# Performance work log

Hardware: AMD Instinct MI355X
Metric: run time of the kernel (lower is better)

## Reference

```python
import jax, jax.numpy as jnp
import numpy as np
from jax import lax

C = 128      # channels
H = 128
W = 128
B = 2
WS = 4       # window size
HEADS = 4
HID = int(C * 2.66)  # 340
EPS = 1e-6


def conv1x1(x, w):
    # x: [b,c,h,w], w: [out,in]
    return jnp.einsum('oc,bchw->bohw', w, x)


def dwconv3(x, w):
    # depthwise 3x3, w: [c,1,3,3]
    return lax.conv_general_dilated(
        x, w, window_strides=(1, 1), padding='SAME',
        feature_group_count=x.shape[1],
        dimension_numbers=('NCHW', 'OIHW', 'NCHW'))


def layernorm(x, w, b):
    # channel-wise LN over dim 1 (per pixel), w/b: [C]
    m = x.mean(axis=1, keepdims=True)
    v = ((x - m) ** 2).mean(axis=1, keepdims=True)
    xn = (x - m) / jnp.sqrt(v + EPS)
    return xn * w[None, :, None, None] + b[None, :, None, None]


def l2norm(x):
    n = jnp.sqrt(jnp.sum(x * x, axis=-1, keepdims=True))
    return x / jnp.maximum(n, 1e-12)


def rsa(x, qkv_w, dw_w, proj_w, temp):
    b, c, h, w = x.shape
    ws = WS
    x_ = jnp.roll(x, (-ws // 2, -ws // 2), axis=(2, 3))  # shifts > 0
    qkv = dwconv3(conv1x1(x_, qkv_w), dw_w)
    q, k, v = jnp.split(qkv, 3, axis=1)

    def win(t):  # b c (h dh) (w dw) -> b (h w) (dh dw) c
        return t.reshape(b, c, h // ws, ws, w // ws, ws) \
                .transpose(0, 2, 4, 3, 5, 1) \
                .reshape(b, (h // ws) * (w // ws), ws * ws, c)

    q, k, v = win(q), win(k), win(v)
    q = l2norm(q)
    k = l2norm(k)
    # attn = q^T @ k  -> [b, nw, c, c]
    attn = jax.nn.relu(jnp.einsum('bnpc,bnpd->bncd', q, k) * temp[0, 0, 0])
    out = jnp.einsum('bnpc,bncd->bnpd', v, attn)  # v @ attn
    out = out.reshape(b, h // ws, w // ws, ws, ws, c) \
             .transpose(0, 5, 1, 3, 2, 4).reshape(b, c, h, w)
    out = jnp.roll(out, (ws // 2, ws // 2), axis=(2, 3))
    return conv1x1(out, proj_w)


def gsa(x, qkv_w, dw_w, proj_w, temp):
    b, c, h, w = x.shape
    hd = HEADS
    ch = c // hd
    qkv = dwconv3(conv1x1(x, qkv_w), dw_w)
    q, k, v = jnp.split(qkv, 3, axis=1)

    def hs(t):  # b (head c) h w -> b head c (h w)
        return t.reshape(b, hd, ch, h * w)

    q, k, v = hs(q), hs(k), hs(v)
    q = l2norm(q)
    k = l2norm(k)
    attn = jax.nn.relu(jnp.einsum('bhcn,bhdn->bhcd', q, k) * temp[0, 0, 0])
    out = jnp.einsum('bhcd,bhdn->bhcn', attn, v).reshape(b, c, h, w)
    return conv1x1(out, proj_w)


def ffn(x, w_in, w_dw, w_out):
    h = dwconv3(conv1x1(x, w_in), w_dw)
    h = jax.nn.gelu(h, approximate=False)
    return conv1x1(h, w_out)


def setup_inputs() -> dict:
    key = jax.random.key(0)
    ks = jax.random.split(key, 16)
    s = 0.05
    d = {
        'x': jax.random.normal(ks[0], (B, C, H, W), jnp.float32),
        # spatial (RSA) branch
        'w_s0': jnp.ones((C,), jnp.float32), 'b_s0': jnp.zeros((C,), jnp.float32),
        'w_s2': jnp.ones((C,), jnp.float32), 'b_s2': jnp.zeros((C,), jnp.float32),
        'rsa_qkv': jax.random.normal(ks[1], (3 * C, C), jnp.float32) * s,
        'rsa_dw': jax.random.normal(ks[2], (3 * C, 1, 3, 3), jnp.float32) * s,
        'rsa_proj': jax.random.normal(ks[3], (C, C), jnp.float32) * s,
        'rsa_temp': jnp.ones((1, 1, 1), jnp.float32),
        'ffs_in': jax.random.normal(ks[4], (HID, C), jnp.float32) * s,
        'ffs_dw': jax.random.normal(ks[5], (HID, 1, 3, 3), jnp.float32) * s,
        'ffs_out': jax.random.normal(ks[6], (C, HID), jnp.float32) * s,
        # channel (GSA) branch
        'w_c0': jnp.ones((C,), jnp.float32), 'b_c0': jnp.zeros((C,), jnp.float32),
        'w_c2': jnp.ones((C,), jnp.float32), 'b_c2': jnp.zeros((C,), jnp.float32),
        'gsa_qkv': jax.random.normal(ks[7], (3 * C, C), jnp.float32) * s,
        'gsa_dw': jax.random.normal(ks[8], (3 * C, 1, 3, 3), jnp.float32) * s,
        'gsa_proj': jax.random.normal(ks[9], (C, C), jnp.float32) * s,
        'gsa_temp': jnp.ones((1, 1, 1), jnp.float32),
        'ffc_in': jax.random.normal(ks[10], (HID, C), jnp.float32) * s,
        'ffc_dw': jax.random.normal(ks[11], (HID, 1, 3, 3), jnp.float32) * s,
        'ffc_out': jax.random.normal(ks[12], (C, HID), jnp.float32) * s,
    }
    return d


def reference(x, w_s0, b_s0, w_s2, b_s2, rsa_qkv, rsa_dw, rsa_proj, rsa_temp,
              ffs_in, ffs_dw, ffs_out,
              w_c0, b_c0, w_c2, b_c2, gsa_qkv, gsa_dw, gsa_proj, gsa_temp,
              ffc_in, ffc_dw, ffc_out):
    # shared_depth = 1: only the i==0 branches execute
    # spatial block (RSA)
    x_ = rsa(layernorm(x, w_s0, b_s0), rsa_qkv, rsa_dw, rsa_proj, rsa_temp)
    x = ffn(layernorm(x_ + x, w_s2, b_s2), ffs_in, ffs_dw, ffs_out) + x_
    # channel block (GSA)
    x_ = gsa(layernorm(x, w_c0, b_c0), gsa_qkv, gsa_dw, gsa_proj, gsa_temp)
    x = ffn(layernorm(x_ + x, w_c2, b_c2), ffc_in, ffc_dw, ffc_out) + x_
    return x
```

## Files before the change

### kernel.cpp

```cpp
#include <hip/hip_runtime.h>
#include <hip/hip_bf16.h>
#include <math.h>

typedef __hip_bfloat16 bf16;
typedef __attribute__((ext_vector_type(8))) short short8;
typedef __attribute__((ext_vector_type(4))) short short4v;
typedef __attribute__((ext_vector_type(4))) float float4v;

static constexpr int cB  = 2;
static constexpr int cC  = 128;
static constexpr int cH  = 128;
static constexpr int cW  = 128;
static constexpr int cP  = cH * cW;
static constexpr int cC3 = 384;
static constexpr int cHID = 340;
static constexpr int cNW = 1024;
static constexpr float cEPS = 1e-6f;

__device__ __forceinline__ float bfu2f(unsigned short u){
  union { unsigned int i; float f; } c; c.i = ((unsigned int)u) << 16; return c.f;
}
__device__ __forceinline__ unsigned short f2b(float f){
  union { float f; unsigned int u; } c; c.f = f;
  unsigned int r = c.u + 0x7FFFu + ((c.u >> 16) & 1u);
  return (unsigned short)(r >> 16);
}

__global__ void k_wcvt(const float* __restrict__ qkv_s, const float* __restrict__ qkv_c,
                       const float* __restrict__ fin_s, const float* __restrict__ fin_c,
                       const float* __restrict__ prj_s, const float* __restrict__ prj_c,
                       const float* __restrict__ fo_s,  const float* __restrict__ fo_c,
                       unsigned short* __restrict__ WB, float* __restrict__ S){
  int i = blockIdx.x * 256 + threadIdx.x;
  if (i >= 319488){
    int j = i - 319488;
    if (j < 8704) S[j] = 0.f;
    return;
  }
  float v;
  if (i < 98304){
    v = (i < 49152) ? qkv_s[i] : qkv_c[i - 49152];
  } else if (i < 196608){
    int j = (i < 147456) ? (i - 98304) : (i - 147456);
    int row = j >> 7, col = j & 127;
    const float* src = (i < 147456) ? fin_s : fin_c;
    v = (row < cHID) ? src[row * 128 + col] : 0.f;
  } else if (i < 229376){
    v = (i < 212992) ? prj_s[i - 196608] : prj_c[i - 212992];
  } else {
    int j = (i < 274432) ? (i - 229376) : (i - 274432);
    int row = j / 352, col = j - row * 352;
    const float* src = (i < 274432) ? fo_s : fo_c;
    v = (col < cHID) ? src[row * cHID + col] : 0.f;
  }
  WB[i] = f2b(v);
}

__global__ void __launch_bounds__(256) k_ln(const float* __restrict__ a,
                                            const float* __restrict__ gamma,
                                            const float* __restrict__ beta,
                                            unsigned short* __restrict__ out, int sh, int sw){
  int idx = blockIdx.x * 256 + threadIdx.x;
  if (idx >= cB * cP) return;
  int b = idx >> 14;
  int p = idx & (cP - 1);
  const float* ap = a + (size_t)b * cC * cP + p;
  float s = 0.f, ss = 0.f;
  #pragma unroll 8
  for (int c = 0; c < cC; c++){
    float v = ap[c * cP];
    s += v; ss += v * v;
  }
  float m = s * (1.f / cC);
  float var = ss * (1.f / cC) - m * m;
  float rstd = rsqrtf(var + cEPS);
  int h = p >> 7, w = p & 127;
  int h2 = (h + sh) & (cH - 1);
  int w2 = (w + sw) & (cW - 1);
  unsigned short* op = out + (size_t)b * cP * cC + (size_t)(h2 * cW + w2) * cC;
  #pragma unroll
  for (int c8 = 0; c8 < cC; c8 += 8){
    short8 tv;
    #pragma unroll
    for (int j = 0; j < 8; j++){
      float v = ap[(c8 + j) * cP];
      tv[j] = (short)f2b((v - m) * rstd * gamma[c8 + j] + beta[c8 + j]);
    }
    *(short8*)(op + c8) = tv;
  }
}

__global__ void __launch_bounds__(256) k_gemm(const unsigned short* __restrict__ Wb,
                                              const unsigned short* __restrict__ Xg,
                                              unsigned short* __restrict__ Out,
                                              int K, int PK, int PM){
  __shared__ short SMEM[8704];
  short* Wls = SMEM;
  short* Xls = SMEM + 5120;
  int bid = blockIdx.x;
  int s  = (bid & 7) * (1536 >> 3) + (bid >> 3);
  int mt = s % 3;
  int r3 = s / 3;
  int pt = r3 & 255;
  int b  = r3 >> 8;
  int p0 = pt * 64;
  int m0 = mt * 128;
  int t  = threadIdx.x;
  int lanelo = t & 15;
  int quad   = (t >> 4) & 3;
  int wv = t >> 6;
  int w1 = wv & 1;
  int w2 = wv >> 1;
  int srw = t >> 1;
  int kow = (t & 1) * 16;
  int srx = t >> 2;
  int kox = (t & 3) * 8;

  float4v acc[2][4];
  #pragma unroll
  for (int i = 0; i < 2; i++)
    #pragma unroll
    for (int j = 0; j < 4; j++)
      acc[i][j] = (float4v){0.f, 0.f, 0.f, 0.f};

  const unsigned short* Xb = Xg + (size_t)b * cP * PK;

  for (int k0 = 0; k0 < K; k0 += 32){
    short8 xv  = *(const short8*)(Xb + (size_t)(p0 + srx) * PK + k0 + kox);
    short8 wv0 = *(const short8*)(Wb + (size_t)(m0 + srw) * K + k0 + kow);
    short8 wv1 = *(const short8*)(Wb + (size_t)(m0 + srw) * K + k0 + kow + 8);
    __syncthreads();
    *(short8*)&Wls[srw * 40 + kow]     = wv0;
    *(short8*)&Wls[srw * 40 + kow + 8] = wv1;
    *(short8*)&Xls[srx * 40 + kox]     = xv;
    __syncthreads();
    short8 af[2], bfr[4];
    #pragma unroll
    for (int i = 0; i < 2; i++)
      af[i] = *(const short8*)&Xls[(w1 * 32 + i * 16 + lanelo) * 40 + quad * 8];
    #pragma unroll
    for (int j = 0; j < 4; j++)
      bfr[j] = *(const short8*)&Wls[(w2 * 64 + j * 16 + lanelo) * 40 + quad * 8];
    #pragma unroll
    for (int i = 0; i < 2; i++)
      #pragma unroll
      for (int j = 0; j < 4; j++)
        acc[i][j] = __builtin_amdgcn_mfma_f32_16x16x32_bf16(af[i], bfr[j], acc[i][j], 0, 0, 0);
  }
  __syncthreads();
  #pragma unroll
  for (int i = 0; i < 2; i++)
    #pragma unroll
    for (int j = 0; j < 4; j++){
      int pixloc = w1 * 32 + i * 16 + quad * 4;
      int mloc   = w2 * 64 + j * 16 + lanelo;
      #pragma unroll
      for (int r = 0; r < 4; r++)
        SMEM[(pixloc + r) * 136 + mloc] = (short)f2b(acc[i][j][r]);
    }
  __syncthreads();
  unsigned short* Ob = Out + (size_t)b * cP * PM;
  #pragma unroll
  for (int rr = 0; rr < 4; rr++){
    int id = t + rr * 256;
    int row = id >> 4, col8 = (id & 15) * 8;
    int wcol = m0 + col8;
    if (wcol < PM)
      *(short8*)(Ob + (size_t)(p0 + row) * PM + wcol) = *(const short8*)&SMEM[row * 136 + col8];
  }
}

template<int MODE>
__global__ void __launch_bounds__(256) k_gemm64(const unsigned short* __restrict__ Wb,
                                                const unsigned short* __restrict__ Xg,
                                                const float* __restrict__ R,
                                                const float* __restrict__ Base,
                                                const float* __restrict__ gamma,
                                                const float* __restrict__ beta,
                                                float* __restrict__ Tr,
                                                unsigned short* __restrict__ LNo,
                                                int K, int PK){
  __shared__ short SMEM[8704];
  __shared__ float gls[128], bls[128];
  __shared__ float psum[64], pssq[64];
  short* Wls = SMEM;
  short* Xls = SMEM + 5120;
  int b  = blockIdx.z;
  int p0 = blockIdx.x * 64;
  int t  = threadIdx.x;
  int lanelo = t & 15;
  int quad   = (t >> 4) & 3;
  int wv = t >> 6;
  int w2 = wv >> 1, w1 = wv & 1;
  int srw = t >> 1;
  int kow = (t & 1) * 16;
  int srx = t >> 2;
  int kox = (t & 3) * 8;

  if (MODE != 3){
    if (t < 128){ gls[t] = gamma[t]; bls[t] = beta[t]; }
    if (t < 64){ psum[t] = 0.f; pssq[t] = 0.f; }
  }

  float4v acc[4][2];
  #pragma unroll
  for (int i = 0; i < 4; i++){
    acc[i][0] = (float4v){0.f, 0.f, 0.f, 0.f};
    acc[i][1] = (float4v){0.f, 0.f, 0.f, 0.f};
  }
  const unsigned short* Xb = Xg + (size_t)b * cP * PK;

  for (int k0 = 0; k0 < K; k0 += 32){
    short8 xv = *(const short8*)(Xb + (size_t)(p0 + srx) * PK + k0 + kox);
    short8 wv0 = *(const short8*)(Wb + (size_t)srw * K + k0 + kow);
    short8 wv1 = *(const short8*)(Wb + (size_t)srw * K + k0 + kow + 8);
    __syncthreads();
    *(short8*)&Wls[srw * 40 + kow]     = wv0;
    *(short8*)&Wls[srw * 40 + kow + 8] = wv1;
    *(short8*)&Xls[srx * 40 + kox]     = xv;
    __syncthreads();
    short8 af[4], bfr[2];
    #pragma unroll
    for (int i = 0; i < 4; i++)
      af[i] = *(const short8*)&Wls[(w2 * 64 + i * 16 + lanelo) * 40 + quad * 8];
    #pragma unroll
    for (int j = 0; j < 2; j++)
      bfr[j] = *(const short8*)&Xls[(w1 * 32 + j * 16 + lanelo) * 40 + quad * 8];
    #pragma unroll
    for (int i = 0; i < 4; i++)
      #pragma unroll
      for (int j = 0; j < 2; j++)
        acc[i][j] = __builtin_amdgcn_mfma_f32_16x16x32_bf16(af[i], bfr[j], acc[i][j], 0, 0, 0);
  }
  float lnv[4][2][4];
  #pragma unroll
  for (int i = 0; i < 4; i++)
    #pragma unroll
    for (int j = 0; j < 2; j++){
      int n = p0 + w1 * 32 + j * 16 + lanelo;
      #pragma unroll
      for (int r = 0; r < 4; r++){
        int m = w2 * 64 + i * 16 + quad * 4 + r;
        size_t idx = (size_t)b * cC * cP + (size_t)m * cP + n;
        float v = acc[i][j][r];
        if (MODE >= 2) v += R[idx];
        Tr[idx] = v;
        if (MODE == 1) v += Base[idx];
        lnv[i][j][r] = v;
      }
    }
  if (MODE == 3) return;
  __syncthreads();
  #pragma unroll
  for (int j = 0; j < 2; j++){
    int nl = w1 * 32 + j * 16 + lanelo;
    float s = 0.f, ss = 0.f;
    #pragma unroll
    for (int i = 0; i < 4; i++)
      #pragma unroll
      for (int r = 0; r < 4; r++){
        float v = lnv[i][j][r];
        s += v; ss += v * v;
      }
    atomicAdd(&psum[nl], s);
    atomicAdd(&pssq[nl], ss);
  }
  __syncthreads();
  #pragma unroll
  for (int j = 0; j < 2; j++){
    int nl = w1 * 32 + j * 16 + lanelo;
    float mean = psum[nl] * (1.f / cC);
    float var = pssq[nl] * (1.f / cC) - mean * mean;
    float rstd = rsqrtf(var + cEPS);
    #pragma unroll
    for (int i = 0; i < 4; i++)
      #pragma unroll
      for (int r = 0; r < 4; r++){
        int m = w2 * 64 + i * 16 + quad * 4 + r;
        SMEM[nl * 136 + m] = (short)f2b((lnv[i][j][r] - mean) * rstd * gls[m] + bls[m]);
      }
  }
  __syncthreads();
  unsigned short* Ob = LNo + (size_t)b * cP * cC;
  #pragma unroll
  for (int rr = 0; rr < 4; rr++){
    int id = t + rr * 256;
    int row = id >> 4, col8 = (id & 15) * 8;
    short8 sv = *(const short8*)&SMEM[row * 136 + col8];
    *(short8*)(Ob + (size_t)(p0 + row) * cC + col8) = sv;
  }
}

template<int GELU, int CCn, int PITCH>
__global__ void __launch_bounds__(256) k_dw(const unsigned short* __restrict__ in,
                                            const float* __restrict__ wt,
                                            unsigned short* __restrict__ out){
  __shared__ float wls[16 * 76];
  int t = threadIdx.x;
  int cbase = blockIdx.y * 128;
  for (int i = t; i < 16 * 72; i += 256){
    int cg = i / 72, rem = i - cg * 72;
    int tap = rem >> 3, j = rem & 7;
    int c = cbase + cg * 8 + j;
    wls[cg * 76 + rem] = (c < CCn) ? wt[c * 9 + tap] : 0.f;
  }
  __syncthreads();
  int cgl = t & 15, pixl = t >> 4;
  int c0 = cbase + cgl * 8;
  if (c0 >= PITCH) return;
  int p = blockIdx.x * 16 + pixl;
  int h = p >> 7, w = p & 127;
  int b = blockIdx.z;
  const unsigned short* ib = in + (size_t)b * cP * PITCH;
  float4 wreg[18];
  #pragma unroll
  for (int q = 0; q < 18; q++)
    wreg[q] = *(const float4*)&wls[cgl * 76 + q * 4];
  short8 v[9];
  #pragma unroll
  for (int ky = 0; ky < 3; ky++){
    int hh = h + ky - 1;
    bool okh = (unsigned)hh < (unsigned)cH;
    int hc = okh ? hh : h;
    #pragma unroll
    for (int kx = 0; kx < 3; kx++){
      int ww = w + kx - 1;
      bool okw = (unsigned)ww < (unsigned)cW;
      int wc = okw ? ww : w;
      short8 lv = *(const short8*)(ib + (size_t)(hc * cW + wc) * PITCH + c0);
      if (!(okh && okw)) lv = (short8){0,0,0,0,0,0,0,0};
      v[ky * 3 + kx] = lv;
    }
  }
  float acc[8] = {0,0,0,0,0,0,0,0};
  #pragma unroll
  for (int tap = 0; tap < 9; tap++){
    float4 w0 = wreg[tap * 2];
    float4 w1 = wreg[tap * 2 + 1];
    float wa[8] = {w0.x, w0.y, w0.z, w0.w, w1.x, w1.y, w1.z, w1.w};
    #pragma unroll
    for (int j = 0; j < 8; j++)
      acc[j] += wa[j] * bfu2f((unsigned short)v[tap][j]);
  }
  short8 ov;
  #pragma unroll
  for (int j = 0; j < 8; j++){
    float vv = acc[j];
    if (GELU) vv = 0.5f * vv * (1.f + erff(vv * 0.70710678118654752f));
    ov[j] = (short)f2b(vv);
  }
  *(short8*)(out + (size_t)b * cP * PITCH + (size_t)p * PITCH + c0) = ov;
}

__global__ void __launch_bounds__(256) k_rsa(const unsigned short* __restrict__ qkv,
                                             const float* __restrict__ temp,
                                             unsigned short* __restrict__ out){
  constexpr int QT = 0;
  constexpr int KT = 5120;
  constexpr int VO = 10240;
  constexpr int AT = 12416;
  __shared__ short lds[21632];
  __shared__ float nq[16], nk[16];
  int blk = blockIdx.x;
  int b  = blk >> 10;
  int nw = blk & 1023;
  int hb = nw >> 5, wb = nw & 31;
  int t = threadIdx.x;
  #pragma unroll
  for (int j = 0; j < 5; j++)
    *(short8*)&lds[t * 40 + j * 8] = (short8){0,0,0,0,0,0,0,0};
  if (t < 16) nq[t] = 0.f;
  else if (t < 32) nk[t - 16] = 0.f;
  __syncthreads();
  const unsigned short* base = qkv + (size_t)b * cP * cC3;
  #pragma unroll
  for (int r = 0; r < 3; r++){
    int i = t + 256 * r;
    int pix = i / 48;
    int cg = i - pix * 48;
    int c0 = cg * 8;
    int gp = (hb * 4 + (pix >> 2)) * cW + wb * 4 + (pix & 3);
    short8 v = *(const short8*)(base + (size_t)gp * cC3 + c0);
    if (c0 < 256){
      float s = 0.f;
      #pragma unroll
      for (int e = 0; e < 8; e++){ float f = bfu2f((unsigned short)v[e]); s += f * f; }
      int off = (c0 < 128) ? (QT + c0 * 40) : (KT + (c0 - 128) * 40);
      #pragma unroll
      for (int e = 0; e < 8; e++) lds[off + e * 40 + pix] = v[e];
      atomicAdd((c0 < 128) ? &nq[pix] : &nk[pix], s);
    } else {
      *(short8*)&lds[VO + pix * 136 + (c0 - 256)] = v;
    }
  }
  __syncthreads();
  float T = temp[0];
  #pragma unroll
  for (int r = 0; r < 8; r++){
    int idx = t + 256 * r;
    int c = idx >> 4, p = idx & 15;
    float sc = (1.f / fmaxf(sqrtf(nq[p]), 1e-12f)) * (1.f / fmaxf(sqrtf(nk[p]), 1e-12f));
    int a = QT + c * 40 + p;
    lds[a] = (short)f2b(bfu2f((unsigned short)lds[a]) * sc);
  }
  __syncthreads();
  int lanelo = t & 15;
  int quad = (t >> 4) & 3;
  int wv = t >> 6;
  float4v oacc[2];
  oacc[0] = (float4v){0.f,0.f,0.f,0.f};
  oacc[1] = (float4v){0.f,0.f,0.f,0.f};
  for (int ch = 0; ch < 2; ch++){
    #pragma unroll
    for (int ct = 0; ct < 4; ct++){
      int c0 = ch * 64 + ct * 16;
      short8 af = *(const short8*)&lds[QT + (c0 + lanelo) * 40 + quad * 8];
      #pragma unroll
      for (int dt = 0; dt < 2; dt++){
        int d0 = wv * 32 + dt * 16;
        short8 bf = *(const short8*)&lds[KT + (d0 + lanelo) * 40 + quad * 8];
        float4v acc = __builtin_amdgcn_mfma_f32_16x16x32_bf16(af, bf,
                        (float4v){0.f,0.f,0.f,0.f}, 0, 0, 0);
        short4v sv;
        #pragma unroll
        for (int r2 = 0; r2 < 4; r2++) sv[r2] = (short)f2b(fmaxf(acc[r2] * T, 0.f));
        *(short4v*)&lds[AT + (d0 + lanelo) * 72 + ct * 16 + quad * 4] = sv;
      }
    }
    __syncthreads();
    #pragma unroll
    for (int dt = 0; dt < 2; dt++){
      int d0 = wv * 32 + dt * 16;
      #pragma unroll
      for (int kk = 0; kk < 2; kk++){
        short8 av8 = *(const short8*)&lds[VO + lanelo * 136 + ch * 64 + kk * 32 + quad * 8];
        short8 bv8 = *(const short8*)&lds[AT + (d0 + lanelo) * 72 + kk * 32 + quad * 8];
        oacc[dt] = __builtin_amdgcn_mfma_f32_16x16x32_bf16(av8, bv8, oacc[dt], 0, 0, 0);
      }
    }
    __syncthreads();
  }
  #pragma unroll
  for (int dt = 0; dt < 2; dt++){
    int d = wv * 32 + dt * 16 + lanelo;
    #pragma unroll
    for (int r2 = 0; r2 < 4; r2++){
      int p = quad * 4 + r2;
      lds[p * 136 + d] = (short)f2b(oacc[dt][r2]);
    }
  }
  __syncthreads();
  {
    int px = t >> 4, cg = (t & 15) * 8;
    int h2 = (hb * 4 + (px >> 2) + 2) & (cH - 1);
    int w2 = (wb * 4 + (px & 3) + 2) & (cW - 1);
    short8 sv = *(const short8*)&lds[px * 136 + cg];
    *(short8*)(out + (size_t)b * cP * cC + (size_t)(h2 * cW + w2) * cC + cg) = sv;
  }
}

__global__ void __launch_bounds__(256) k_gram(const unsigned short* __restrict__ qkv,
                                              float* __restrict__ S,
                                              float* __restrict__ Qn,
                                              float* __restrict__ Kn){
  __shared__ float qs[32][132];
  __shared__ float ks[32][132];
  int blk = blockIdx.x;
  int chunk = blk & 127;
  int bh = blk >> 7;
  int b = bh >> 2, hd = bh & 3;
  int n0 = chunk * 128;
  int t = threadIdx.x;
  {
    int row = t >> 1;
    int half = t & 1;
    const unsigned short* pq = qkv + (size_t)b * cP * cC3 + (size_t)(n0 + row) * cC3 + hd * 32 + half * 16;
    const unsigned short* pk = pq + 128;
    short8 q0 = *(const short8*)pq;
    short8 q1 = *(const short8*)(pq + 8);
    short8 k0 = *(const short8*)pk;
    short8 k1 = *(const short8*)(pk + 8);
    #pragma unroll
    for (int e = 0; e < 8; e++){
      qs[half * 16 + e][row]     = bfu2f((unsigned short)q0[e]);
      qs[half * 16 + 8 + e][row] = bfu2f((unsigned short)q1[e]);
      ks[half * 16 + e][row]     = bfu2f((unsigned short)k0[e]);
      ks[half * 16 + 8 + e][row] = bfu2f((unsigned short)k1[e]);
    }
  }
  __syncthreads();
  if (t < 64){
    const float* row = (t < 32) ? qs[t] : ks[t - 32];
    float s = 0.f;
    #pragma unroll
    for (int i = 0; i < 128; i += 4){
      float4 v = *(const float4*)(row + i);
      s += v.x*v.x + v.y*v.y + v.z*v.z + v.w*v.w;
    }
    if (t < 32) atomicAdd(&Qn[bh * 32 + t], s);
    else        atomicAdd(&Kn[bh * 32 + (t - 32)], s);
  }
  int cc = (t >> 4) * 2;
  int dd = t & 15;
  float a00 = 0.f, a01 = 0.f, a10 = 0.f, a11 = 0.f;
  for (int n = 0; n < 128; n += 4){
    float4 q0 = *(const float4*)&qs[cc][n];
    float4 q1 = *(const float4*)&qs[cc + 1][n];
    float4 k0 = *(const float4*)&ks[dd][n];
    float4 k1 = *(const float4*)&ks[dd + 16][n];
    a00 += q0.x*k0.x + q0.y*k0.y + q0.z*k0.z + q0.w*k0.w;
    a01 += q0.x*k1.x + q0.y*k1.y + q0.z*k1.z + q0.w*k1.w;
    a10 += q1.x*k0.x + q1.y*k0.y + q1.z*k0.z + q1.w*k0.w;
    a11 += q1.x*k1.x + q1.y*k1.y + q1.z*k1.z + q1.w*k1.w;
  }
  float* Sb = S + (size_t)bh * 1024;
  atomicAdd(&Sb[cc * 32 + dd], a00);
  atomicAdd(&Sb[cc * 32 + dd + 16], a01);
  atomicAdd(&Sb[(cc + 1) * 32 + dd], a10);
  atomicAdd(&Sb[(cc + 1) * 32 + dd + 16], a11);
}

__global__ void __launch_bounds__(256) k_applyM(const unsigned short* __restrict__ qkv,
                                                const float* __restrict__ S,
                                                const float* __restrict__ Qn,
                                                const float* __restrict__ Kn,
                                                const float* __restrict__ temp,
                                                unsigned short* __restrict__ out){
  __shared__ short atb[128 * 40];
  __shared__ short OT[64 * 136];
  int b = blockIdx.y;
  int nbase = blockIdx.x * 64;
  int t = threadIdx.x;
  float T = temp[0];
  #pragma unroll
  for (int it = 0; it < 16; it++){
    int i = t + it * 256;
    int c = i >> 5, d = i & 31;
    int hd = c >> 5, cl = c & 31;
    int bh = b * 4 + hd;
    float nqv = fmaxf(sqrtf(Qn[bh * 32 + cl]), 1e-12f);
    float nkv = fmaxf(sqrtf(Kn[bh * 32 + d]), 1e-12f);
    float v = fmaxf(S[(size_t)bh * 1024 + cl * 32 + d] / (nqv * nkv) * T, 0.f);
    atb[c * 40 + d] = (short)f2b(v);
  }
  __syncthreads();
  int lanelo = t & 15, quad = (t >> 4) & 3, wv = t >> 6;
  int n0 = nbase + wv * 16;
  const unsigned short* vb = qkv + (size_t)b * cP * cC3 + (size_t)(n0 + lanelo) * cC3 + 256 + quad * 8;
  #pragma unroll
  for (int hd = 0; hd < 4; hd++){
    short8 af = *(const short8*)(vb + hd * 32);
    #pragma unroll
    for (int cth = 0; cth < 2; cth++){
      int c0 = hd * 32 + cth * 16;
      short8 bf = *(const short8*)&atb[(c0 + lanelo) * 40 + quad * 8];
      float4v acc = __builtin_amdgcn_mfma_f32_16x16x32_bf16(af, bf,
                      (float4v){0.f,0.f,0.f,0.f}, 0, 0, 0);
      #pragma unroll
      for (int r = 0; r < 4; r++)
        OT[(wv * 16 + quad * 4 + r) * 136 + c0 + lanelo] = (short)f2b(acc[r]);
    }
  }
  __syncthreads();
  unsigned short* ob = out + (size_t)b * cP * cC;
  #pragma unroll
  for (int rr = 0; rr < 4; rr++){
    int id = t + rr * 256;
    int row = id >> 4, col8 = (id & 15) * 8;
    *(short8*)(ob + (size_t)(nbase + row) * cC + col8) = *(const short8*)&OT[row * 136 + col8];
  }
}

extern "C" void kernel_launch(void* const* d_in, const int* in_sizes, int n_in,
                              void* d_out, int out_size, void* d_ws, size_t ws_size,
                              hipStream_t stream){
  const float* x     = (const float*)d_in[0];
  const float* w_s0  = (const float*)d_in[1];
  const float* b_s0  = (const float*)d_in[2];
  const float* w_s2  = (const float*)d_in[3];
  const float* b_s2  = (const float*)d_in[4];
  const float* rsa_qkv  = (const float*)d_in[5];
  const float* rsa_dw   = (const float*)d_in[6];
  const float* rsa_proj = (const float*)d_in[7];
  const float* rsa_temp = (const float*)d_in[8];
  const float* ffs_in   = (const float*)d_in[9];
  const float* ffs_dw   = (const float*)d_in[10];
  const float* ffs_out  = (const float*)d_in[11];
  const float* w_c0  = (const float*)d_in[12];
  const float* b_c0  = (const float*)d_in[13];
  const float* w_c2  = (const float*)d_in[14];
  const float* b_c2  = (const float*)d_in[15];
  const float* gsa_qkv  = (const float*)d_in[16];
  const float* gsa_dw   = (const float*)d_in[17];
  const float* gsa_proj = (const float*)d_in[18];
  const float* gsa_temp = (const float*)d_in[19];
  const float* ffc_in   = (const float*)d_in[20];
  const float* ffc_dw   = (const float*)d_in[21];
  const float* ffc_out  = (const float*)d_in[22];

  const size_t szC  = (size_t)cB * cC * cP;
  const size_t szC3 = (size_t)cB * cC3 * cP;
  float* XF = (float*)d_ws;
  float* XS = XF + szC;
  unsigned short* LO   = (unsigned short*)(XS + szC);
  unsigned short* Abuf = LO + szC;
  unsigned short* Bbuf = Abuf + szC3;
  float* S  = (float*)(Bbuf + szC3);
  float* Qn = S + 8192;
  float* Kn = Qn + 256;
  float* AT = Kn + 256;
  unsigned short* WB = (unsigned short*)(AT + 1024);
  unsigned short* W_QKV_S = WB;
  unsigned short* W_QKV_C = WB + 49152;
  unsigned short* W_FIN_S = WB + 98304;
  unsigned short* W_FIN_C = WB + 147456;
  unsigned short* W_PRJ_S = WB + 196608;
  unsigned short* W_PRJ_C = WB + 212992;
  unsigned short* W_FO_S  = WB + 229376;
  unsigned short* W_FO_C  = WB + 274432;

  dim3 t256(256);
  dim3 gLN(cB * cP / 256);
  dim3 gG1(cP / 64 * 3 * cB);
  dim3 gG64(cP / 64, 1, cB);
  dim3 gDW(cP / 16, 3, cB);

  k_wcvt<<<dim3(1282), t256, 0, stream>>>(rsa_qkv, gsa_qkv, ffs_in, ffc_in,
                                          rsa_proj, gsa_proj, ffs_out, ffc_out, WB, S);

  k_ln<<<gLN, t256, 0, stream>>>(x, w_s0, b_s0, LO, 126, 126);
  k_gemm<<<gG1, t256, 0, stream>>>(W_QKV_S, LO, Abuf, 128, 128, 384);
  k_dw<0,384,384><<<gDW, t256, 0, stream>>>(Abuf, rsa_dw, Bbuf);
  k_rsa<<<dim3(cB * cNW), t256, 0, stream>>>(Bbuf, rsa_temp, LO);
  k_gemm64<1><<<gG64, t256, 0, stream>>>(W_PRJ_S, LO, nullptr, x, w_s2, b_s2, XS, LO, 128, 128);
  k_gemm<<<gG1, t256, 0, stream>>>(W_FIN_S, LO, Abuf, 128, 128, 352);
  k_dw<1,340,352><<<gDW, t256, 0, stream>>>(Abuf, ffs_dw, Bbuf);
  k_gemm64<2><<<gG64, t256, 0, stream>>>(W_FO_S, Bbuf, XS, nullptr, w_c0, b_c0, XF, LO, 352, 352);

  k_gemm<<<gG1, t256, 0, stream>>>(W_QKV_C, LO, Abuf, 128, 128, 384);
  k_dw<0,384,384><<<gDW, t256, 0, stream>>>(Abuf, gsa_dw, Bbuf);
  k_gram<<<dim3(1024), t256, 0, stream>>>(Bbuf, S, Qn, Kn);
  k_applyM<<<dim3(cP / 64, cB), t256, 0, stream>>>(Bbuf, S, Qn, Kn, gsa_temp, LO);
  k_gemm64<1><<<gG64, t256, 0, stream>>>(W_PRJ_C, LO, nullptr, XF, w_c2, b_c2, XS, LO, 128, 128);
  k_gemm<<<gG1, t256, 0, stream>>>(W_FIN_C, LO, Abuf, 128, 128, 352);
  k_dw<1,340,352><<<gDW, t256, 0, stream>>>(Abuf, ffc_dw, Bbuf);
  k_gemm64<3><<<gG64, t256, 0, stream>>>(W_FO_C, Bbuf, XS, nullptr, nullptr, nullptr,
                                         (float*)d_out, nullptr, 352, 352);
}
```

Measured before the change: 365.0 us.

## Fuse first LayerNorm into QKV GEMM and prefetch next K-slice in GEMMs

Replaces the standalone LayerNorm kernel with a fused kernel that reads fp32 input, computes per-pixel LN stats via shared-memory atomics, writes normalized bf16 directly into LDS, and runs the QKV GEMM from there with the roll shift applied on the read side. This removes one launch and the bf16 intermediate round-trip through global memory, at the cost of recomputing LN three times (once per M tile). Separately, the generic GEMM kernels now issue global loads for the next K-slice before the MFMA work on the current one, a register-level software prefetch meant to hide load latency.

```diff
diff --git a/kernel.cpp b/kernel.cpp
--- a/kernel.cpp
+++ b/kernel.cpp
@@ -56,37 +56,111 @@
   WB[i] = f2b(v);
 }
 
-__global__ void __launch_bounds__(256) k_ln(const float* __restrict__ a,
-                                            const float* __restrict__ gamma,
-                                            const float* __restrict__ beta,
-                                            unsigned short* __restrict__ out, int sh, int sw){
-  int idx = blockIdx.x * 256 + threadIdx.x;
-  if (idx >= cB * cP) return;
-  int b = idx >> 14;
-  int p = idx & (cP - 1);
-  const float* ap = a + (size_t)b * cC * cP + p;
-  float s = 0.f, ss = 0.f;
-  #pragma unroll 8
-  for (int c = 0; c < cC; c++){
-    float v = ap[c * cP];
-    s += v; ss += v * v;
-  }
-  float m = s * (1.f / cC);
-  float var = ss * (1.f / cC) - m * m;
+__global__ void __launch_bounds__(256) k_gemmLN(const unsigned short* __restrict__ Wb,
+                                                const float* __restrict__ Xf,
+                                                const float* __restrict__ gamma,
+                                                const float* __restrict__ beta,
+                                                unsigned short* __restrict__ Out){
+  __shared__ short Xls[64 * 136];
+  __shared__ short Wls[128 * 40];
+  __shared__ float gls[128], bls[128];
+  __shared__ float psum[64], pssq[64];
+  int bid = blockIdx.x;
+  int s  = (bid & 7) * 192 + (bid >> 3);
+  int mt = s % 3;
+  int r3 = s / 3;
+  int pt = r3 & 255;
+  int b  = r3 >> 8;
+  int p0 = pt * 64;
+  int m0 = mt * 128;
+  int t  = threadIdx.x;
+  int px = t & 63, cq = t >> 6;
+  if (t < 64){ psum[t] = 0.f; pssq[t] = 0.f; }
+  if (t < 128){ gls[t] = gamma[t]; bls[t] = beta[t]; }
+  int rh = p0 >> 7, w0 = p0 & 127;
+  int hs = (rh + 2) & (cH - 1);
+  int sp = hs * cW + ((w0 + 2 + px) & (cW - 1));
+  const float* xb = Xf + (size_t)b * cC * cP + sp;
+  float xr[32];
+  float s1 = 0.f, s2 = 0.f;
+  #pragma unroll
+  for (int j = 0; j < 32; j++){
+    float v = xb[(size_t)(cq * 32 + j) * cP];
+    xr[j] = v; s1 += v; s2 += v * v;
+  }
+  __syncthreads();
+  atomicAdd(&psum[px], s1);
+  atomicAdd(&pssq[px], s2);
+  __syncthreads();
+  float mean = psum[px] * (1.f / cC);
+  float var  = pssq[px] * (1.f / cC) - mean * mean;
   float rstd = rsqrtf(var + cEPS);
-  int h = p >> 7, w = p & 127;
-  int h2 = (h + sh) & (cH - 1);
-  int w2 = (w + sw) & (cW - 1);
-  unsigned short* op = out + (size_t)b * cP * cC + (size_t)(h2 * cW + w2) * cC;
-  #pragma unroll
-  for (int c8 = 0; c8 < cC; c8 += 8){
+  #pragma unroll
+  for (int k = 0; k < 4; k++){
     short8 tv;
     #pragma unroll
-    for (int j = 0; j < 8; j++){
-      float v = ap[(c8 + j) * cP];
-      tv[j] = (short)f2b((v - m) * rstd * gamma[c8 + j] + beta[c8 + j]);
-    }
-    *(short8*)(op + c8) = tv;
+    for (int e = 0; e < 8; e++){
+      int c = cq * 32 + k * 8 + e;
+      tv[e] = (short)f2b((xr[k * 8 + e] - mean) * rstd * gls[c] + bls[c]);
+    }
+    *(short8*)&Xls[px * 136 + cq * 32 + k * 8] = tv;
+  }
+  int lanelo = t & 15;
+  int quad   = (t >> 4) & 3;
+  int wv = t >> 6;
+  int w1 = wv & 1;
+  int w2 = wv >> 1;
+  int srw = t >> 1;
+  int kow = (t & 1) * 16;
+  float4v acc[2][4];
+  #pragma unroll
+  for (int i = 0; i < 2; i++)
+    #pragma unroll
+    for (int j = 0; j < 4; j++)
+      acc[i][j] = (float4v){0.f, 0.f, 0.f, 0.f};
+  const unsigned short* Wp = Wb + (size_t)(m0 + srw) * 128 + kow;
+  short8 a0 = *(const short8*)(Wp);
+  short8 a1 = *(const short8*)(Wp + 8);
+  for (int k0 = 0; k0 < 128; k0 += 32){
+    __syncthreads();
+    *(short8*)&Wls[srw * 40 + kow]     = a0;
+    *(short8*)&Wls[srw * 40 + kow + 8] = a1;
+    __syncthreads();
+    if (k0 < 96){
+      a0 = *(const short8*)(Wp + k0 + 32);
+      a1 = *(const short8*)(Wp + k0 + 40);
+    }
+    short8 af[2], bfr[4];
+    #pragma unroll
+    for (int i = 0; i < 2; i++)
+      af[i] = *(const short8*)&Xls[(w1 * 32 + i * 16 + lanelo) * 136 + k0 + quad * 8];
+    #pragma unroll
+    for (int j = 0; j < 4; j++)
+      bfr[j] = *(const short8*)&Wls[(w2 * 64 + j * 16 + lanelo) * 40 + quad * 8];
+    #pragma unroll
+    for (int i = 0; i < 2; i++)
+      #pragma unroll
+      for (int j = 0; j < 4; j++)
+        acc[i][j] = __builtin_amdgcn_mfma_f32_16x16x32_bf16(af[i], bfr[j], acc[i][j], 0, 0, 0);
+  }
+  __syncthreads();
+  #pragma unroll
+  for (int i = 0; i < 2; i++)
+    #pragma unroll
+    for (int j = 0; j < 4; j++){
+      int pixloc = w1 * 32 + i * 16 + quad * 4;
+      int mloc   = w2 * 64 + j * 16 + lanelo;
+      #pragma unroll
+      for (int r = 0; r < 4; r++)
+        Xls[(pixloc + r) * 136 + mloc] = (short)f2b(acc[i][j][r]);
+    }
+  __syncthreads();
+  unsigned short* Ob = Out + (size_t)b * cP * cC3;
+  #pragma unroll
+  for (int rr = 0; rr < 4; rr++){
+    int id = t + rr * 256;
+    int row = id >> 4, col8 = (id & 15) * 8;
+    *(short8*)(Ob + (size_t)(p0 + row) * cC3 + m0 + col8) = *(const short8*)&Xls[row * 136 + col8];
   }
 }
 
@@ -123,17 +197,23 @@
     for (int j = 0; j < 4; j++)
       acc[i][j] = (float4v){0.f, 0.f, 0.f, 0.f};
 
-  const unsigned short* Xb = Xg + (size_t)b * cP * PK;
-
+  const unsigned short* Xp = Xg + (size_t)b * cP * PK + (size_t)(p0 + srx) * PK + kox;
+  const unsigned short* Wp = Wb + (size_t)(m0 + srw) * K + kow;
+
+  short8 xv  = *(const short8*)(Xp);
+  short8 wv0 = *(const short8*)(Wp);
+  short8 wv1 = *(const short8*)(Wp + 8);
   for (int k0 = 0; k0 < K; k0 += 32){
-    short8 xv  = *(const short8*)(Xb + (size_t)(p0 + srx) * PK + k0 + kox);
-    short8 wv0 = *(const short8*)(Wb + (size_t)(m0 + srw) * K + k0 + kow);
-    short8 wv1 = *(const short8*)(Wb + (size_t)(m0 + srw) * K + k0 + kow + 8);
     __syncthreads();
     *(short8*)&Wls[srw * 40 + kow]     = wv0;
     *(short8*)&Wls[srw * 40 + kow + 8] = wv1;
     *(short8*)&Xls[srx * 40 + kox]     = xv;
     __syncthreads();
+    if (k0 + 32 < K){
+      xv  = *(const short8*)(Xp + k0 + 32);
+      wv0 = *(const short8*)(Wp + k0 + 32);
+      wv1 = *(const short8*)(Wp + k0 + 40);
+    }
     short8 af[2], bfr[4];
     #pragma unroll
     for (int i = 0; i < 2; i++)
@@ -208,17 +288,23 @@
     acc[i][0] = (float4v){0.f, 0.f, 0.f, 0.f};
     acc[i][1] = (float4v){0.f, 0.f, 0.f, 0.f};
   }
-  const unsigned short* Xb = Xg + (size_t)b * cP * PK;
-
+  const unsigned short* Xp = Xg + (size_t)b * cP * PK + (size_t)(p0 + srx) * PK + kox;
+  const unsigned short* Wp = Wb + (size_t)srw * K + kow;
+
+  short8 xv  = *(const short8*)(Xp);
+  short8 wv0 = *(const short8*)(Wp);
+  short8 wv1 = *(const short8*)(Wp + 8);
   for (int k0 = 0; k0 < K; k0 += 32){
-    short8 xv = *(const short8*)(Xb + (size_t)(p0 + srx) * PK + k0 + kox);
-    short8 wv0 = *(const short8*)(Wb + (size_t)srw * K + k0 + kow);
-    short8 wv1 = *(const short8*)(Wb + (size_t)srw * K + k0 + kow + 8);
     __syncthreads();
     *(short8*)&Wls[srw * 40 + kow]     = wv0;
     *(short8*)&Wls[srw * 40 + kow + 8] = wv1;
     *(short8*)&Xls[srx * 40 + kox]     = xv;
     __syncthreads();
+    if (k0 + 32 < K){
+      xv  = *(const short8*)(Xp + k0 + 32);
+      wv0 = *(const short8*)(Wp + k0 + 32);
+      wv1 = *(const short8*)(Wp + k0 + 40);
+    }
     short8 af[4], bfr[2];
     #pragma unroll
     for (int i = 0; i < 4; i++)
@@ -620,7 +706,6 @@
   unsigned short* W_FO_C  = WB + 274432;
 
   dim3 t256(256);
-  dim3 gLN(cB * cP / 256);
   dim3 gG1(cP / 64 * 3 * cB);
   dim3 gG64(cP / 64, 1, cB);
   dim3 gDW(cP / 16, 3, cB);
@@ -628,8 +713,7 @@
   k_wcvt<<<dim3(1282), t256, 0, stream>>>(rsa_qkv, gsa_qkv, ffs_in, ffc_in,
                                           rsa_proj, gsa_proj, ffs_out, ffc_out, WB, S);
 
-  k_ln<<<gLN, t256, 0, stream>>>(x, w_s0, b_s0, LO, 126, 126);
-  k_gemm<<<gG1, t256, 0, stream>>>(W_QKV_S, LO, Abuf, 128, 128, 384);
+  k_gemmLN<<<gG1, t256, 0, stream>>>(W_QKV_S, x, w_s0, b_s0, Abuf);
   k_dw<0,384,384><<<gDW, t256, 0, stream>>>(Abuf, rsa_dw, Bbuf);
   k_rsa<<<dim3(cB * cNW), t256, 0, stream>>>(Bbuf, rsa_temp, LO);
   k_gemm64<1><<<gG64, t256, 0, stream>>>(W_PRJ_S, LO, nullptr, x, w_s2, b_s2, XS, LO, 128, 128);
```

Measured after the change: 349.3 us. 4.3% less time.
